# Performance work log

Measured on AMD Instinct MI355X. Metric: run time of the kernel, lower is better.

Reference implementation:

```python
import jax, jax.numpy as jnp
import numpy as np

EMBED = 1024
HEADS = 16
HEAD_DIM = EMBED // HEADS
B, S = 4, 2048


def setup_inputs() -> dict:
    key = jax.random.key(0)
    ks = jax.random.split(key, 9)
    inp = {
        "values": jax.random.normal(ks[0], (B, S, EMBED), jnp.float32),
        "keys": jax.random.normal(ks[1], (B, S, EMBED), jnp.float32),
        "queries": jax.random.normal(ks[2], (B, S, EMBED), jnp.float32),
        "mask": jax.random.randint(ks[3], (B, 1, S, S), 0, 2, jnp.int32),
        # nn.Linear(head_dim, head_dim, bias=False) weights, stored torch-style (out, in)
        "Wv": jax.random.normal(ks[4], (HEAD_DIM, HEAD_DIM), jnp.float32) / np.sqrt(HEAD_DIM),
        "Wk": jax.random.normal(ks[5], (HEAD_DIM, HEAD_DIM), jnp.float32) / np.sqrt(HEAD_DIM),
        "Wq": jax.random.normal(ks[6], (HEAD_DIM, HEAD_DIM), jnp.float32) / np.sqrt(HEAD_DIM),
        # fc_out: Linear(heads*head_dim, embed_size) with bias
        "Wo": jax.random.normal(ks[7], (EMBED, EMBED), jnp.float32) / np.sqrt(EMBED),
        "bo": jax.random.normal(ks[8], (EMBED,), jnp.float32) * 0.01,
    }
    return inp


def reference(values, keys, queries, mask, Wv, Wk, Wq, Wo, bo):
    N, q_len = queries.shape[0], queries.shape[1]
    v_len, k_len = values.shape[1], keys.shape[1]
    # split heads: (N, len, H, Dh)
    v = values.reshape(N, v_len, HEADS, HEAD_DIM)
    k = keys.reshape(N, k_len, HEADS, HEAD_DIM)
    q = queries.reshape(N, q_len, HEADS, HEAD_DIM)
    # per-head linear projections (torch Linear: x @ W^T)
    v = jnp.einsum("nlhd,ed->nlhe", v, Wv)
    k = jnp.einsum("nlhd,ed->nlhe", k, Wk)
    q = jnp.einsum("nlhd,ed->nlhe", q, Wq)
    # scores (N, H, q_len, k_len)
    energy = jnp.einsum("nqhd,nkhd->nhqk", q, k)
    energy = jnp.where(mask == 0, jnp.float32(-1e20), energy)
    # NOTE: original scales by sqrt(embed_size), not sqrt(head_dim)
    attention = jax.nn.softmax(energy / np.sqrt(EMBED).astype(np.float32), axis=3)
    out = jnp.einsum("nhql,nlhd->nqhd", attention, v).reshape(N, q_len, EMBED)
    return out @ Wo.T + bo
```

## Files before the change

### kernel.cpp

```cpp
#include <hip/hip_runtime.h>
#include <hip/hip_bf16.h>

#define S_LEN 2048
#define NHEAD 16
#define DHEAD 64
#define EMB   1024
#define NB    4
#define KBLK  64
#define NT    (S_LEN / KBLK)

typedef short s16x8 __attribute__((ext_vector_type(8)));
typedef float f32x4 __attribute__((ext_vector_type(4)));

#define MFMA16(a, b, c) __builtin_amdgcn_mfma_f32_16x16x32_bf16(a, b, c, 0, 0, 0)

#if __has_builtin(__builtin_amdgcn_exp2f)
#define EXP2(x) __builtin_amdgcn_exp2f(x)
#else
#define EXP2(x) exp2f(x)
#endif

__device__ inline unsigned short f2bf(float f) {
    return __builtin_bit_cast(unsigned short, __float2bfloat16(f));
}

__device__ inline s16x8 cvt8(const float* __restrict__ p) {
    const f32x4* q = (const f32x4*)p;
    f32x4 a = q[0], b = q[1];
    s16x8 r;
    r[0] = (short)f2bf(a[0]); r[1] = (short)f2bf(a[1]);
    r[2] = (short)f2bf(a[2]); r[3] = (short)f2bf(a[3]);
    r[4] = (short)f2bf(b[0]); r[5] = (short)f2bf(b[1]);
    r[6] = (short)f2bf(b[2]); r[7] = (short)f2bf(b[3]);
    return r;
}

__global__ __launch_bounds__(256) void cvt_wo(const float* __restrict__ Wo,
                                              unsigned short* __restrict__ Wb) {
    int i = (blockIdx.x * 256 + threadIdx.x) * 4;
    f32x4 v = *(const f32x4*)(Wo + i);
    unsigned long long pk = (unsigned long long)f2bf(v[0])
                          | ((unsigned long long)f2bf(v[1]) << 16)
                          | ((unsigned long long)f2bf(v[2]) << 32)
                          | ((unsigned long long)f2bf(v[3]) << 48);
    *(unsigned long long*)(Wb + i) = pk;
}

__global__ __launch_bounds__(256) void packmask(const int* __restrict__ mask,
                                                unsigned long long* __restrict__ Mp) {
    int wid0 = (blockIdx.x * 4 + ((int)threadIdx.x >> 6)) * 16;
    int lane = threadIdx.x & 63;
    #pragma unroll 8
    for (int i = 0; i < 16; ++i) {
        size_t w = (size_t)wid0 + i;
        int m = mask[w * 64 + lane];
        unsigned long long bal = __ballot(m != 0);
        if (lane == 0) Mp[w] = bal;
    }
}

__global__ __launch_bounds__(256) void projqk(const float* __restrict__ x,
                                              const unsigned short* __restrict__ W3,
                                              unsigned short* __restrict__ out,
                                              float scale) {
    int wave = threadIdx.x >> 6, lane = threadIdx.x & 63;
    int g = lane >> 4, c = lane & 15;
    int m0 = (blockIdx.x * 4 + wave) * 16;

    s16x8 a0 = cvt8(x + (size_t)(m0 + c) * 64 + g * 8);
    s16x8 a1 = cvt8(x + (size_t)(m0 + c) * 64 + 32 + g * 8);

    const f32x4 fzero = {0.f, 0.f, 0.f, 0.f};
    f32x4 acc[4];
    #pragma unroll
    for (int nt = 0; nt < 4; ++nt) {
        s16x8 b0 = *(const s16x8*)(W3 + (size_t)(nt * 16 + c) * 64 + g * 8);
        s16x8 b1 = *(const s16x8*)(W3 + (size_t)(nt * 16 + c) * 64 + 32 + g * 8);
        f32x4 z = fzero;
        z = MFMA16(a0, b0, z);
        z = MFMA16(a1, b1, z);
        acc[nt] = z;
    }
    #pragma unroll
    for (int j = 0; j < 4; ++j) {
        int m = m0 + g * 4 + j;
        int h = m & 15, s = (m >> 4) & (S_LEN - 1), b = m >> 15;
        #pragma unroll
        for (int nt = 0; nt < 4; ++nt) {
            int col = nt * 16 + c;
            out[((size_t)((b * NHEAD + h) * S_LEN + s)) * DHEAD + col] = f2bf(acc[nt][j] * scale);
        }
    }
}

__global__ __launch_bounds__(256) void projv(const float* __restrict__ x,
                                             const unsigned short* __restrict__ W3,
                                             unsigned short* __restrict__ Vt) {
    int wave = threadIdx.x >> 6, lane = threadIdx.x & 63;
    int g = lane >> 4, c = lane & 15;
    int s0 = blockIdx.x * 64;
    int bh = blockIdx.y, b = bh >> 4, h = bh & 15;
    int m0 = wave * 16;

    s16x8 a0 = *(const s16x8*)(W3 + (size_t)(m0 + c) * 64 + g * 8);
    s16x8 a1 = *(const s16x8*)(W3 + (size_t)(m0 + c) * 64 + 32 + g * 8);

    const f32x4 fzero = {0.f, 0.f, 0.f, 0.f};
    f32x4 acc[4];
    #pragma unroll
    for (int nt = 0; nt < 4; ++nt) {
        int s = s0 + nt * 16 + c;
        const float* xr = x + ((size_t)(b * S_LEN + s) * NHEAD + h) * DHEAD;
        s16x8 b0 = cvt8(xr + g * 8);
        s16x8 b1 = cvt8(xr + 32 + g * 8);
        f32x4 z = fzero;
        z = MFMA16(a0, b0, z);
        z = MFMA16(a1, b1, z);
        acc[nt] = z;
    }
    #pragma unroll
    for (int j = 0; j < 4; ++j) {
        int e = m0 + g * 4 + j;
        unsigned short* Vr = Vt + ((size_t)(bh * DHEAD) + e) * S_LEN;
        #pragma unroll
        for (int nt = 0; nt < 4; ++nt) {
            Vr[s0 + nt * 16 + c] = f2bf(acc[nt][j]);
        }
    }
}

__global__ __launch_bounds__(256, 3) void attn(const unsigned short* __restrict__ Qp,
                                               const unsigned short* __restrict__ Kp,
                                               const unsigned short* __restrict__ Vt,
                                               const unsigned long long* __restrict__ Mp,
                                               unsigned short* __restrict__ Oa) {
    __shared__ unsigned short Kl[2][8][64][8];
    __shared__ unsigned short Vl[2][8][64][8];
    __shared__ unsigned short Pl[4][2][16 * 72];

    int tid = threadIdx.x;
    int wave = tid >> 6, lane = tid & 63, g = lane >> 4, c = lane & 15;
    int bid = blockIdx.x;
    int xcd = bid & 7, idx = bid >> 3;
    int bh = xcd * 8 + (idx >> 4);
    int qblk = idx & 15;
    int b = bh >> 4, h = bh & 15;
    int q0 = qblk * 128 + wave * 32;

    const unsigned short* Qb = Qp + (size_t)bh * S_LEN * DHEAD;
    const unsigned short* Kb = Kp + (size_t)bh * S_LEN * DHEAD;
    const unsigned short* Vb = Vt + (size_t)bh * DHEAD * S_LEN;
    const unsigned long long* mb = Mp + (size_t)b * S_LEN * NT;

    s16x8 aq[2][2];
    #pragma unroll
    for (int mi = 0; mi < 2; ++mi) {
        aq[mi][0] = *(const s16x8*)(Qb + (size_t)(q0 + mi * 16 + c) * 64 + g * 8);
        aq[mi][1] = *(const s16x8*)(Qb + (size_t)(q0 + mi * 16 + c) * 64 + 32 + g * 8);
    }

    int cid = tid * 2;
    int kr = cid >> 3, kch = cid & 7;
    const unsigned short* Ksrc = Kb + (size_t)kr * 64 + kch * 8;
    const unsigned short* Vsrc = Vb + (size_t)kr * S_LEN + kch * 8;
    unsigned short* Kd0 = &Kl[0][(kr >> 4) * 2 + (kch >> 2)][(kch & 3) * 16 + (kr & 15)][0];
    unsigned short* Kd1 = &Kl[0][(kr >> 4) * 2 + ((kch + 1) >> 2)][((kch + 1) & 3) * 16 + (kr & 15)][0];
    unsigned short* Vd0 = &Vl[0][(kr >> 4) * 2 + (kch >> 2)][(kch & 3) * 16 + (kr & 15)][0];
    unsigned short* Vd1 = &Vl[0][(kr >> 4) * 2 + ((kch + 1) >> 2)][((kch + 1) & 3) * 16 + (kr & 15)][0];

    const f32x4 fzero = {0.f, 0.f, 0.f, 0.f};
    f32x4 acc[2][4], accl[2];
    #pragma unroll
    for (int mi = 0; mi < 2; ++mi) {
        accl[mi] = fzero;
        #pragma unroll
        for (int nt = 0; nt < 4; ++nt) acc[mi][nt] = fzero;
    }
    s16x8 ones;
    #pragma unroll
    for (int i = 0; i < 8; ++i) ones[i] = (short)0x3F80;

    s16x8 gk0, gk1, gv0, gv1;
    auto LOADR = [&](int kt) {
        size_t k0 = (size_t)kt * KBLK;
        gk0 = *(const s16x8*)(Ksrc + k0 * 64);
        gk1 = *(const s16x8*)(Ksrc + k0 * 64 + 8);
        gv0 = *(const s16x8*)(Vsrc + k0);
        gv1 = *(const s16x8*)(Vsrc + k0 + 8);
    };
    auto STAGEW = [&](int bufv) {
        int off = bufv * 4096;
        *(s16x8*)(Kd0 + off) = gk0;
        *(s16x8*)(Kd1 + off) = gk1;
        *(s16x8*)(Vd0 + off) = gv0;
        *(s16x8*)(Vd1 + off) = gv1;
    };

    auto COMPUTE = [&](int bufv, int kt) {
        unsigned long long mw[2][4];
        #pragma unroll
        for (int mi = 0; mi < 2; ++mi)
            #pragma unroll
            for (int j = 0; j < 4; ++j)
                mw[mi][j] = mb[(size_t)(q0 + mi * 16 + g * 4 + j) * NT + kt];

        f32x4 sc[2][4];
        #pragma unroll
        for (int nt = 0; nt < 4; ++nt) {
            s16x8 kf0 = *(const s16x8*)&Kl[bufv][nt * 2][lane][0];
            s16x8 kf1 = *(const s16x8*)&Kl[bufv][nt * 2 + 1][lane][0];
            #pragma unroll
            for (int mi = 0; mi < 2; ++mi) {
                f32x4 z = MFMA16(aq[mi][0], kf0, fzero);
                sc[mi][nt] = MFMA16(aq[mi][1], kf1, z);
            }
        }
        #pragma unroll
        for (int mi = 0; mi < 2; ++mi) {
            unsigned short* Pw = &Pl[wave][mi][0];
            #pragma unroll
            for (int j = 0; j < 4; ++j) {
                unsigned wlo = (unsigned)mw[mi][j];
                unsigned whi = (unsigned)(mw[mi][j] >> 32);
                int r = g * 4 + j;
                #pragma unroll
                for (int nt = 0; nt < 4; ++nt) {
                    float e = EXP2(sc[mi][nt][j]);
                    unsigned part = (nt < 2) ? wlo : whi;
                    float p = e * (float)((part >> ((nt & 1) * 16 + c)) & 1u);
                    Pw[r * 72 + nt * 16 + c] = f2bf(p);
                }
            }
        }
        s16x8 ap[2][2];
        #pragma unroll
        for (int mi = 0; mi < 2; ++mi) {
            const unsigned short* Pw = &Pl[wave][mi][0];
            ap[mi][0] = *(const s16x8*)(Pw + c * 72 + g * 8);
            ap[mi][1] = *(const s16x8*)(Pw + c * 72 + 32 + g * 8);
            accl[mi] = MFMA16(ap[mi][0], ones, accl[mi]);
            accl[mi] = MFMA16(ap[mi][1], ones, accl[mi]);
        }
        #pragma unroll
        for (int nt = 0; nt < 4; ++nt) {
            s16x8 vf0 = *(const s16x8*)&Vl[bufv][nt * 2][lane][0];
            s16x8 vf1 = *(const s16x8*)&Vl[bufv][nt * 2 + 1][lane][0];
            #pragma unroll
            for (int mi = 0; mi < 2; ++mi) {
                acc[mi][nt] = MFMA16(ap[mi][0], vf0, acc[mi][nt]);
                acc[mi][nt] = MFMA16(ap[mi][1], vf1, acc[mi][nt]);
            }
        }
    };

    LOADR(0);
    STAGEW(0);
    __syncthreads();
    for (int kt = 0; kt < NT; ++kt) {
        int cur = kt & 1;
        if (kt + 1 < NT) LOADR(kt + 1);
        COMPUTE(cur, kt);
        __syncthreads();
        if (kt + 1 < NT) {
            STAGEW(cur ^ 1);
            __syncthreads();
        }
    }

    #pragma unroll
    for (int mi = 0; mi < 2; ++mi)
        #pragma unroll
        for (int j = 0; j < 4; ++j) {
            int q = q0 + mi * 16 + g * 4 + j;
            float inv = 1.f / accl[mi][j];
            #pragma unroll
            for (int nt = 0; nt < 4; ++nt)
                Oa[((size_t)(b * S_LEN + q)) * EMB + h * DHEAD + nt * 16 + c] = f2bf(acc[mi][nt][j] * inv);
        }
}

__global__ __launch_bounds__(256, 2) void outproj(const unsigned short* __restrict__ A,
                                                  const unsigned short* __restrict__ Wb,
                                                  const float* __restrict__ bo,
                                                  float* __restrict__ out) {
    int wave = threadIdx.x >> 6, lane = threadIdx.x & 63;
    int g = lane >> 4, c = lane & 15;
    int bid = blockIdx.x;
    int xcd = bid & 7, idx = bid >> 3;
    int bx = xcd * 4 + (idx >> 4);
    int by = idx & 15;
    int r0 = bx * 256 + wave * 64;
    int n0 = by * 64;

    float bias[4];
    #pragma unroll
    for (int nt = 0; nt < 4; ++nt) bias[nt] = bo[n0 + nt * 16 + c];

    const f32x4 fzero = {0.f, 0.f, 0.f, 0.f};
    f32x4 acc[4][4];
    #pragma unroll
    for (int mi = 0; mi < 4; ++mi)
        #pragma unroll
        for (int nt = 0; nt < 4; ++nt) acc[mi][nt] = fzero;

    s16x8 aA[4], bA[4], aB[4], bB[4];
    auto LOADT = [&](s16x8 (&a)[4], s16x8 (&bw)[4], int kt) {
        int kb = kt * 32;
        #pragma unroll
        for (int mi = 0; mi < 4; ++mi)
            a[mi] = *(const s16x8*)(A + (size_t)(r0 + mi * 16 + c) * EMB + kb + g * 8);
        #pragma unroll
        for (int nt = 0; nt < 4; ++nt)
            bw[nt] = *(const s16x8*)(Wb + (size_t)(n0 + nt * 16 + c) * EMB + kb + g * 8);
    };
    auto MM = [&](s16x8 (&a)[4], s16x8 (&bw)[4]) {
        #pragma unroll
        for (int mi = 0; mi < 4; ++mi)
            #pragma unroll
            for (int nt = 0; nt < 4; ++nt)
                acc[mi][nt] = MFMA16(a[mi], bw[nt], acc[mi][nt]);
    };

    LOADT(aA, bA, 0);
    for (int kt = 0; kt < EMB / 32; kt += 2) {
        LOADT(aB, bB, kt + 1);
        MM(aA, bA);
        if (kt + 2 < EMB / 32) LOADT(aA, bA, kt + 2);
        MM(aB, bB);
    }

    #pragma unroll
    for (int mi = 0; mi < 4; ++mi)
        #pragma unroll
        for (int j = 0; j < 4; ++j) {
            int row = r0 + mi * 16 + g * 4 + j;
            #pragma unroll
            for (int nt = 0; nt < 4; ++nt)
                out[(size_t)row * EMB + n0 + nt * 16 + c] = acc[mi][nt][j] + bias[nt];
        }
}

extern "C" void kernel_launch(void* const* d_in, const int* in_sizes, int n_in,
                              void* d_out, int out_size, void* d_ws, size_t ws_size,
                              hipStream_t stream) {
    (void)in_sizes; (void)n_in; (void)out_size; (void)ws_size;
    const float* values  = (const float*)d_in[0];
    const float* keys    = (const float*)d_in[1];
    const float* queries = (const float*)d_in[2];
    const int*   mask    = (const int*)d_in[3];
    const float* Wv = (const float*)d_in[4];
    const float* Wk = (const float*)d_in[5];
    const float* Wq = (const float*)d_in[6];
    const float* Wo = (const float*)d_in[7];
    const float* bo = (const float*)d_in[8];
    float* out = (float*)d_out;

    unsigned short* Qp = (unsigned short*)d_ws;
    unsigned short* Kp = Qp + (size_t)8 * 1024 * 1024;
    unsigned short* Vt = Kp + (size_t)8 * 1024 * 1024;
    unsigned short* Oa = Vt + (size_t)8 * 1024 * 1024;
    unsigned short* Wb = Oa + (size_t)8 * 1024 * 1024;
    unsigned long long* Mp = (unsigned long long*)(Wb + (size_t)1024 * 1024);
    unsigned short* Wq3 = (unsigned short*)(Mp + (size_t)262144);
    unsigned short* Wk3 = Wq3 + 4096;
    unsigned short* Wv3 = Wk3 + 4096;

    const float QSCALE = 0.045084220027780106f;

    cvt_wo<<<1024, 256, 0, stream>>>(Wo, Wb);
    cvt_wo<<<4, 256, 0, stream>>>(Wq, Wq3);
    cvt_wo<<<4, 256, 0, stream>>>(Wk, Wk3);
    cvt_wo<<<4, 256, 0, stream>>>(Wv, Wv3);
    packmask<<<4096, 256, 0, stream>>>(mask, Mp);
    projqk<<<2048, 256, 0, stream>>>(queries, Wq3, Qp, QSCALE);
    projqk<<<2048, 256, 0, stream>>>(keys,    Wk3, Kp, 1.0f);
    projv<<<dim3(32, 64), 256, 0, stream>>>(values, Wv3, Vt);
    attn<<<1024, 256, 0, stream>>>(Qp, Kp, Vt, Mp, Oa);
    outproj<<<512, 256, 0, stream>>>(Oa, Wb, bo, out);
}
```

Measured before the change: 423.7 us.

## Merge prep kernels into fewer launches and swizzle attention LDS layouts

Merges the four weight-conversion launches into one kernel and folds mask packing plus the Q, K and V projections into a single launch that picks its work from blockIdx.y. This cuts the launch count from eight prep kernels to two. Inside the attention kernel, the K/V/P shared-memory tiles get an XOR-swizzled flat layout instead of padded or plain indexing, aimed at avoiding LDS bank conflicts. The P buffer shrinks to one 16-row tile per wave, reused per mi, and the occupancy hint rises from 3 to 4 blocks per CU. The larger occupancy target may add register pressure.

```diff
diff --git a/kernel.cpp b/kernel.cpp
--- a/kernel.cpp
+++ b/kernel.cpp
@@ -5,7 +5,6 @@
 #define NHEAD 16
 #define DHEAD 64
 #define EMB   1024
-#define NB    4
 #define KBLK  64
 #define NT    (S_LEN / KBLK)
 
@@ -35,42 +34,101 @@
     return r;
 }
 
-__global__ __launch_bounds__(256) void cvt_wo(const float* __restrict__ Wo,
-                                              unsigned short* __restrict__ Wb) {
-    int i = (blockIdx.x * 256 + threadIdx.x) * 4;
-    f32x4 v = *(const f32x4*)(Wo + i);
+__global__ __launch_bounds__(256) void cvt_weights(const float* __restrict__ Wo,
+                                                   const float* __restrict__ Wq,
+                                                   const float* __restrict__ Wk,
+                                                   const float* __restrict__ Wv,
+                                                   unsigned short* __restrict__ Wb,
+                                                   unsigned short* __restrict__ Wq3,
+                                                   unsigned short* __restrict__ Wk3,
+                                                   unsigned short* __restrict__ Wv3) {
+    int bid = blockIdx.x;
+    const float* src; unsigned short* dst; int base;
+    if (bid < 1024)      { src = Wo; dst = Wb;  base = bid; }
+    else if (bid < 1028) { src = Wq; dst = Wq3; base = bid - 1024; }
+    else if (bid < 1032) { src = Wk; dst = Wk3; base = bid - 1028; }
+    else                 { src = Wv; dst = Wv3; base = bid - 1032; }
+    int i = (base * 256 + threadIdx.x) * 4;
+    f32x4 v = *(const f32x4*)(src + i);
     unsigned long long pk = (unsigned long long)f2bf(v[0])
                           | ((unsigned long long)f2bf(v[1]) << 16)
                           | ((unsigned long long)f2bf(v[2]) << 32)
                           | ((unsigned long long)f2bf(v[3]) << 48);
-    *(unsigned long long*)(Wb + i) = pk;
-}
-
-__global__ __launch_bounds__(256) void packmask(const int* __restrict__ mask,
-                                                unsigned long long* __restrict__ Mp) {
-    int wid0 = (blockIdx.x * 4 + ((int)threadIdx.x >> 6)) * 16;
-    int lane = threadIdx.x & 63;
-    #pragma unroll 8
-    for (int i = 0; i < 16; ++i) {
-        size_t w = (size_t)wid0 + i;
-        int m = mask[w * 64 + lane];
-        unsigned long long bal = __ballot(m != 0);
-        if (lane == 0) Mp[w] = bal;
-    }
-}
-
-__global__ __launch_bounds__(256) void projqk(const float* __restrict__ x,
-                                              const unsigned short* __restrict__ W3,
-                                              unsigned short* __restrict__ out,
-                                              float scale) {
+    *(unsigned long long*)(dst + i) = pk;
+}
+
+__global__ __launch_bounds__(256) void proj4(const float* __restrict__ q_in,
+                                             const float* __restrict__ k_in,
+                                             const float* __restrict__ v_in,
+                                             const int* __restrict__ mask,
+                                             const unsigned short* __restrict__ Wq3,
+                                             const unsigned short* __restrict__ Wk3,
+                                             const unsigned short* __restrict__ Wv3,
+                                             unsigned short* __restrict__ Qp,
+                                             unsigned short* __restrict__ Kp,
+                                             unsigned short* __restrict__ Vt,
+                                             unsigned long long* __restrict__ Mp,
+                                             float qscale) {
+    int mode = blockIdx.y;
     int wave = threadIdx.x >> 6, lane = threadIdx.x & 63;
+    int bid = blockIdx.x;
+
+    if (mode == 3) {
+        int wid0 = (bid * 4 + wave) * 32;
+        #pragma unroll 8
+        for (int i = 0; i < 32; ++i) {
+            size_t w = (size_t)wid0 + i;
+            int m = mask[w * 64 + lane];
+            unsigned long long bal = __ballot(m != 0);
+            if (lane == 0) Mp[w] = bal;
+        }
+        return;
+    }
+
     int g = lane >> 4, c = lane & 15;
-    int m0 = (blockIdx.x * 4 + wave) * 16;
-
+    const f32x4 fzero = {0.f, 0.f, 0.f, 0.f};
+
+    if (mode == 2) {
+        int sblk = bid & 31, bh = bid >> 5;
+        int s0 = sblk * 64;
+        int b = bh >> 4, h = bh & 15;
+        int m0 = wave * 16;
+
+        s16x8 a0 = *(const s16x8*)(Wv3 + (size_t)(m0 + c) * 64 + g * 8);
+        s16x8 a1 = *(const s16x8*)(Wv3 + (size_t)(m0 + c) * 64 + 32 + g * 8);
+
+        f32x4 acc[4];
+        #pragma unroll
+        for (int nt = 0; nt < 4; ++nt) {
+            int s = s0 + nt * 16 + c;
+            const float* xr = v_in + ((size_t)(b * S_LEN + s) * NHEAD + h) * DHEAD;
+            s16x8 b0 = cvt8(xr + g * 8);
+            s16x8 b1 = cvt8(xr + 32 + g * 8);
+            f32x4 z = fzero;
+            z = MFMA16(a0, b0, z);
+            z = MFMA16(a1, b1, z);
+            acc[nt] = z;
+        }
+        #pragma unroll
+        for (int j = 0; j < 4; ++j) {
+            int e = m0 + g * 4 + j;
+            unsigned short* Vr = Vt + ((size_t)(bh * DHEAD) + e) * S_LEN;
+            #pragma unroll
+            for (int nt = 0; nt < 4; ++nt)
+                Vr[s0 + nt * 16 + c] = f2bf(acc[nt][j]);
+        }
+        return;
+    }
+
+    const float* x = (mode == 0) ? q_in : k_in;
+    const unsigned short* W3 = (mode == 0) ? Wq3 : Wk3;
+    unsigned short* out = (mode == 0) ? Qp : Kp;
+    float scale = (mode == 0) ? qscale : 1.0f;
+
+    int m0 = (bid * 4 + wave) * 16;
     s16x8 a0 = cvt8(x + (size_t)(m0 + c) * 64 + g * 8);
     s16x8 a1 = cvt8(x + (size_t)(m0 + c) * 64 + 32 + g * 8);
 
-    const f32x4 fzero = {0.f, 0.f, 0.f, 0.f};
     f32x4 acc[4];
     #pragma unroll
     for (int nt = 0; nt < 4; ++nt) {
@@ -93,50 +151,14 @@
     }
 }
 
-__global__ __launch_bounds__(256) void projv(const float* __restrict__ x,
-                                             const unsigned short* __restrict__ W3,
-                                             unsigned short* __restrict__ Vt) {
-    int wave = threadIdx.x >> 6, lane = threadIdx.x & 63;
-    int g = lane >> 4, c = lane & 15;
-    int s0 = blockIdx.x * 64;
-    int bh = blockIdx.y, b = bh >> 4, h = bh & 15;
-    int m0 = wave * 16;
-
-    s16x8 a0 = *(const s16x8*)(W3 + (size_t)(m0 + c) * 64 + g * 8);
-    s16x8 a1 = *(const s16x8*)(W3 + (size_t)(m0 + c) * 64 + 32 + g * 8);
-
-    const f32x4 fzero = {0.f, 0.f, 0.f, 0.f};
-    f32x4 acc[4];
-    #pragma unroll
-    for (int nt = 0; nt < 4; ++nt) {
-        int s = s0 + nt * 16 + c;
-        const float* xr = x + ((size_t)(b * S_LEN + s) * NHEAD + h) * DHEAD;
-        s16x8 b0 = cvt8(xr + g * 8);
-        s16x8 b1 = cvt8(xr + 32 + g * 8);
-        f32x4 z = fzero;
-        z = MFMA16(a0, b0, z);
-        z = MFMA16(a1, b1, z);
-        acc[nt] = z;
-    }
-    #pragma unroll
-    for (int j = 0; j < 4; ++j) {
-        int e = m0 + g * 4 + j;
-        unsigned short* Vr = Vt + ((size_t)(bh * DHEAD) + e) * S_LEN;
-        #pragma unroll
-        for (int nt = 0; nt < 4; ++nt) {
-            Vr[s0 + nt * 16 + c] = f2bf(acc[nt][j]);
-        }
-    }
-}
-
-__global__ __launch_bounds__(256, 3) void attn(const unsigned short* __restrict__ Qp,
+__global__ __launch_bounds__(256, 4) void attn(const unsigned short* __restrict__ Qp,
                                                const unsigned short* __restrict__ Kp,
                                                const unsigned short* __restrict__ Vt,
                                                const unsigned long long* __restrict__ Mp,
                                                unsigned short* __restrict__ Oa) {
-    __shared__ unsigned short Kl[2][8][64][8];
-    __shared__ unsigned short Vl[2][8][64][8];
-    __shared__ unsigned short Pl[4][2][16 * 72];
+    __shared__ unsigned short Kl[2][4096];
+    __shared__ unsigned short Vl[2][4096];
+    __shared__ unsigned short Pl[4][1024];
 
     int tid = threadIdx.x;
     int wave = tid >> 6, lane = tid & 63, g = lane >> 4, c = lane & 15;
@@ -159,14 +181,20 @@
         aq[mi][1] = *(const s16x8*)(Qb + (size_t)(q0 + mi * 16 + c) * 64 + 32 + g * 8);
     }
 
-    int cid = tid * 2;
-    int kr = cid >> 3, kch = cid & 7;
-    const unsigned short* Ksrc = Kb + (size_t)kr * 64 + kch * 8;
-    const unsigned short* Vsrc = Vb + (size_t)kr * S_LEN + kch * 8;
-    unsigned short* Kd0 = &Kl[0][(kr >> 4) * 2 + (kch >> 2)][(kch & 3) * 16 + (kr & 15)][0];
-    unsigned short* Kd1 = &Kl[0][(kr >> 4) * 2 + ((kch + 1) >> 2)][((kch + 1) & 3) * 16 + (kr & 15)][0];
-    unsigned short* Vd0 = &Vl[0][(kr >> 4) * 2 + (kch >> 2)][(kch & 3) * 16 + (kr & 15)][0];
-    unsigned short* Vd1 = &Vl[0][(kr >> 4) * 2 + ((kch + 1) >> 2)][((kch + 1) & 3) * 16 + (kr & 15)][0];
+    int kr = tid >> 2;
+    int kch0 = (tid & 3) * 2, kch1 = kch0 + 1;
+    const unsigned short* Ksrc = Kb + (size_t)kr * 64 + kch0 * 8;
+    const unsigned short* Vsrc = Vb + (size_t)kr * S_LEN + kch0 * 8;
+    int o0 = ((((kr >> 4) * 2 + (kch0 >> 2)) * 64 + (kch0 & 3) * 16 + (kr & 15)) ^ ((kch0 >> 1) & 3)) * 8;
+    int o1 = ((((kr >> 4) * 2 + (kch1 >> 2)) * 64 + (kch1 & 3) * 16 + (kr & 15)) ^ ((kch1 >> 1) & 3)) * 8;
+    int ro[4][2];
+    #pragma unroll
+    for (int nt = 0; nt < 4; ++nt)
+        #pragma unroll
+        for (int kh = 0; kh < 2; ++kh)
+            ro[nt][kh] = (((nt * 2 + kh) * 64 + lane) ^ ((kh * 2 + (g >> 1)) & 3)) * 8;
+    int po0 = ((c * 8 + g) ^ (c & 7)) * 8;
+    int po1 = ((c * 8 + g + 4) ^ (c & 7)) * 8;
 
     const f32x4 fzero = {0.f, 0.f, 0.f, 0.f};
     f32x4 acc[2][4], accl[2];
@@ -179,6 +207,8 @@
     s16x8 ones;
     #pragma unroll
     for (int i = 0; i < 8; ++i) ones[i] = (short)0x3F80;
+
+    unsigned short* Pw = Pl[wave];
 
     s16x8 gk0, gk1, gv0, gv1;
     auto LOADR = [&](int kt) {
@@ -189,11 +219,10 @@
         gv1 = *(const s16x8*)(Vsrc + k0 + 8);
     };
     auto STAGEW = [&](int bufv) {
-        int off = bufv * 4096;
-        *(s16x8*)(Kd0 + off) = gk0;
-        *(s16x8*)(Kd1 + off) = gk1;
-        *(s16x8*)(Vd0 + off) = gv0;
-        *(s16x8*)(Vd1 + off) = gv1;
+        *(s16x8*)(&Kl[bufv][o0]) = gk0;
+        *(s16x8*)(&Kl[bufv][o1]) = gk1;
+        *(s16x8*)(&Vl[bufv][o0]) = gv0;
+        *(s16x8*)(&Vl[bufv][o1]) = gv1;
     };
 
     auto COMPUTE = [&](int bufv, int kt) {
@@ -207,44 +236,41 @@
         f32x4 sc[2][4];
         #pragma unroll
         for (int nt = 0; nt < 4; ++nt) {
-            s16x8 kf0 = *(const s16x8*)&Kl[bufv][nt * 2][lane][0];
-            s16x8 kf1 = *(const s16x8*)&Kl[bufv][nt * 2 + 1][lane][0];
+            s16x8 kf0 = *(const s16x8*)(&Kl[bufv][ro[nt][0]]);
+            s16x8 kf1 = *(const s16x8*)(&Kl[bufv][ro[nt][1]]);
             #pragma unroll
             for (int mi = 0; mi < 2; ++mi) {
                 f32x4 z = MFMA16(aq[mi][0], kf0, fzero);
                 sc[mi][nt] = MFMA16(aq[mi][1], kf1, z);
             }
         }
+        s16x8 ap[2][2];
         #pragma unroll
         for (int mi = 0; mi < 2; ++mi) {
-            unsigned short* Pw = &Pl[wave][mi][0];
             #pragma unroll
             for (int j = 0; j < 4; ++j) {
                 unsigned wlo = (unsigned)mw[mi][j];
                 unsigned whi = (unsigned)(mw[mi][j] >> 32);
                 int r = g * 4 + j;
+                int rb = r * 8, rx = r & 7;
                 #pragma unroll
                 for (int nt = 0; nt < 4; ++nt) {
                     float e = EXP2(sc[mi][nt][j]);
                     unsigned part = (nt < 2) ? wlo : whi;
                     float p = e * (float)((part >> ((nt & 1) * 16 + c)) & 1u);
-                    Pw[r * 72 + nt * 16 + c] = f2bf(p);
+                    int ph = (rb + nt * 2 + (c >> 3)) ^ rx;
+                    Pw[ph * 8 + (c & 7)] = f2bf(p);
                 }
             }
-        }
-        s16x8 ap[2][2];
-        #pragma unroll
-        for (int mi = 0; mi < 2; ++mi) {
-            const unsigned short* Pw = &Pl[wave][mi][0];
-            ap[mi][0] = *(const s16x8*)(Pw + c * 72 + g * 8);
-            ap[mi][1] = *(const s16x8*)(Pw + c * 72 + 32 + g * 8);
+            ap[mi][0] = *(const s16x8*)(Pw + po0);
+            ap[mi][1] = *(const s16x8*)(Pw + po1);
             accl[mi] = MFMA16(ap[mi][0], ones, accl[mi]);
             accl[mi] = MFMA16(ap[mi][1], ones, accl[mi]);
         }
         #pragma unroll
         for (int nt = 0; nt < 4; ++nt) {
-            s16x8 vf0 = *(const s16x8*)&Vl[bufv][nt * 2][lane][0];
-            s16x8 vf1 = *(const s16x8*)&Vl[bufv][nt * 2 + 1][lane][0];
+            s16x8 vf0 = *(const s16x8*)(&Vl[bufv][ro[nt][0]]);
+            s16x8 vf1 = *(const s16x8*)(&Vl[bufv][ro[nt][1]]);
             #pragma unroll
             for (int mi = 0; mi < 2; ++mi) {
                 acc[mi][nt] = MFMA16(ap[mi][0], vf0, acc[mi][nt]);
@@ -367,14 +393,9 @@
 
     const float QSCALE = 0.045084220027780106f;
 
-    cvt_wo<<<1024, 256, 0, stream>>>(Wo, Wb);
-    cvt_wo<<<4, 256, 0, stream>>>(Wq, Wq3);
-    cvt_wo<<<4, 256, 0, stream>>>(Wk, Wk3);
-    cvt_wo<<<4, 256, 0, stream>>>(Wv, Wv3);
-    packmask<<<4096, 256, 0, stream>>>(mask, Mp);
-    projqk<<<2048, 256, 0, stream>>>(queries, Wq3, Qp, QSCALE);
-    projqk<<<2048, 256, 0, stream>>>(keys,    Wk3, Kp, 1.0f);
-    projv<<<dim3(32, 64), 256, 0, stream>>>(values, Wv3, Vt);
+    cvt_weights<<<1036, 256, 0, stream>>>(Wo, Wq, Wk, Wv, Wb, Wq3, Wk3, Wv3);
+    proj4<<<dim3(2048, 4), 256, 0, stream>>>(queries, keys, values, mask,
+                                             Wq3, Wk3, Wv3, Qp, Kp, Vt, Mp, QSCALE);
     attn<<<1024, 256, 0, stream>>>(Qp, Kp, Vt, Mp, Oa);
     outproj<<<512, 256, 0, stream>>>(Oa, Wb, bo, out);
 }
```

After: 484.8 us. +14.4%, slower.
